# Optimization experiments

Hardware: AMD Instinct MI355X
Metric: run time of the kernel (lower is better)

## Reference

```python
import jax, jax.numpy as jnp
import numpy as np

DIST = 45
HID = 128
NLAYERS = 4
BATCH = 128


def _build_edges(d):
    n = d * d - 1
    sqrt_n = int(np.sqrt(n)) + 1
    src, dst = [], []
    for i in range(n):
        row, col = i // sqrt_n, i % sqrt_n
        for dr, dc in ((-1, 0), (1, 0), (0, -1), (0, 1)):
            nr, nc = row + dr, col + dc
            j = nr * sqrt_n + nc
            if 0 <= nr < sqrt_n and 0 <= j < n and j != i:
                src.append(i)
                dst.append(j)
    return np.asarray(src, np.int32), np.asarray(dst, np.int32), n


def setup_inputs() -> dict:
    key = jax.random.key(0)
    ks = jax.random.split(key, 8)
    src, dst, n = _build_edges(DIST)
    s = 1.0 / np.sqrt(HID)
    return {
        "x": jax.random.normal(ks[0], (BATCH, n), jnp.float32),
        "W_embed": jax.random.normal(ks[1], (1, HID), jnp.float32),
        "b_embed": jnp.zeros((HID,), jnp.float32),
        "gnn_W": jax.random.normal(ks[2], (NLAYERS, 2 * HID, HID), jnp.float32) * s,
        "gnn_b": jnp.zeros((NLAYERS, HID), jnp.float32),
        "ln_g": jnp.ones((NLAYERS, HID), jnp.float32),
        "ln_b": jnp.zeros((NLAYERS, HID), jnp.float32),
        "out_W1": jax.random.normal(ks[3], (HID, HID), jnp.float32) * s,
        "out_b1": jnp.zeros((HID,), jnp.float32),
        "out_W2": jax.random.normal(ks[4], (HID, 2), jnp.float32) * s,
        "out_b2": jnp.zeros((2,), jnp.float32),
        "edge_src": jnp.asarray(src),
        "edge_dst": jnp.asarray(dst),
    }


def _layer_norm(h, g, b, eps=1e-5):
    mu = h.mean(-1, keepdims=True)
    var = ((h - mu) ** 2).mean(-1, keepdims=True)
    return (h - mu) * jax.lax.rsqrt(var + eps) * g + b


def _segment_mean(h, src, dst, n_nodes):
    # h: [B, N, H] -> mean of incoming-neighbor features per node; 0 if no edge.
    hs = jnp.swapaxes(h[:, src, :], 0, 1)                 # [E, B, H]
    sums = jax.ops.segment_sum(hs, dst, num_segments=n_nodes)   # [N, B, H]
    cnt = jax.ops.segment_sum(jnp.ones_like(dst, jnp.float32), dst,
                              num_segments=n_nodes)              # [N]
    agg = jnp.where(cnt[:, None, None] > 0,
                    sums / jnp.maximum(cnt, 1.0)[:, None, None], 0.0)
    return jnp.swapaxes(agg, 0, 1)                        # [B, N, H]


def reference(x, W_embed, b_embed, gnn_W, gnn_b, ln_g, ln_b,
              out_W1, out_b1, out_W2, out_b2, edge_src, edge_dst):
    n_nodes = x.shape[1]
    # node_embed: Linear(1, H) applied to x[..., None]
    h = x[..., None] * W_embed[0] + b_embed               # [B, N, H]
    for l in range(gnn_W.shape[0]):
        agg = _segment_mean(h, edge_src, edge_dst, n_nodes)
        combined = jnp.concatenate([h, agg], axis=-1)     # [B, N, 2H]
        h = jax.nn.relu(combined @ gnn_W[l] + gnn_b[l])
        h = _layer_norm(h, ln_g[l], ln_b[l])
    graph_repr = h.mean(axis=1)                           # [B, H]
    hid = jax.nn.relu(graph_repr @ out_W1 + out_b1)
    return hid @ out_W2 + out_b2                          # [B, 2]
```

## Files before the change

### kernel.cpp

```cpp
#include <hip/hip_runtime.h>

typedef unsigned short u16;
typedef unsigned int   u32;
typedef __attribute__((ext_vector_type(8))) short short8;
typedef __attribute__((ext_vector_type(4))) float f32x4;

#define NN   2024
#define NB   128
#define HID  128
#define MT   128
#define MTOT (NN*NB)
#define NBLK (MTOT/MT)

__device__ __forceinline__ float bflo(u32 w){ union{u32 u; float f;}c; c.u=w<<16;        return c.f; }
__device__ __forceinline__ float bfhi(u32 w){ union{u32 u; float f;}c; c.u=w&0xffff0000u; return c.f; }
__device__ __forceinline__ float bf2f(u16 h){ union{u32 u; float f;}c; c.u=((u32)h)<<16; return c.f; }
__device__ __forceinline__ u16 f2bf(float f){ union{float f; u32 u;}c; c.f=f; return (u16)((c.u+0x7fffu+((c.u>>16)&1u))>>16); }
__device__ __forceinline__ u32 cvtpk(float lo, float hi){
  u32 r; asm("v_cvt_pk_bf16_f32 %0, %1, %2" : "=v"(r) : "v"(lo), "v"(hi)); return r;
}
__device__ __forceinline__ f32x4 mfma16(short8 a, short8 b, f32x4 c){
  return __builtin_amdgcn_mfma_f32_16x16x32_bf16(a,b,c,0,0,0);
}
__device__ __forceinline__ void glds16(const void* g, void* l){
  __builtin_amdgcn_global_load_lds((const __attribute__((address_space(1))) void*)g,
                                   (__attribute__((address_space(3))) void*)l, 16, 0, 0);
}

__device__ __forceinline__ short8 aggc(short8 a0, short8 a1, short8 a2, short8 a3,
                                       float w0, float w1, float w2, float w3){
  union{short8 s; u32 u[4];} A, B, C, D, R;
  A.s=a0; B.s=a1; C.s=a2; D.s=a3;
#pragma unroll
  for (int p=0;p<4;++p){
    float lo = w0*bflo(A.u[p]); lo = fmaf(w1,bflo(B.u[p]),lo); lo = fmaf(w2,bflo(C.u[p]),lo); lo = fmaf(w3,bflo(D.u[p]),lo);
    float hi = w0*bfhi(A.u[p]); hi = fmaf(w1,bfhi(B.u[p]),hi); hi = fmaf(w2,bfhi(C.u[p]),hi); hi = fmaf(w3,bfhi(D.u[p]),hi);
    R.u[p] = cvtpk(lo, hi);
  }
  return R.s;
}

__global__ __launch_bounds__(256, 2)
void layerG_k(const u16* __restrict__ hin, const u16* __restrict__ Wt,
              const float* __restrict__ bias, const float* __restrict__ lng,
              const float* __restrict__ lnb, u16* __restrict__ hout)
{
  __shared__ __align__(16) char lds[65536];
  char* Wl = lds;
  char* Ag = lds + 32768;

  const int t  = threadIdx.x;
  const int l  = t & 63;
  const int wv = t >> 6;
  const int wr = wv >> 1, wc = wv & 1;
  const int cB = l & 15, rg = l >> 4;

  const int orig = blockIdx.x;
  const int m0 = ((orig & 7)*253 + (orig >> 3)) * MT;

  const char* hb = (const char*)hin;

  {
#pragma unroll
    for (int i = 0; i < 8; ++i){
      const int slot = wv*8 + i;
      const int col  = slot*4 + (l >> 4);
      const u32 se   = (u32)col*256 + ((((u32)(l & 15))*8) ^ (((u32)(col & 7))<<3));
      glds16(Wt + se, Wl + (u32)slot*1024);
    }
  }

  const int r  = t >> 1;
  const int hf = t & 1;
  const int grow = m0 + r;
  const int nd = grow % NN;
  const int v0 = (nd >= 45), v1 = (nd <= NN-46), v2 = (nd >= 1), v3 = (nd <= NN-2);
  const int cnt = v0+v1+v2+v3;
  const float inv = (cnt==4) ? 0.25f : ((cnt==3) ? (1.f/3.f) : 0.5f);
  const float w0 = v0 ? inv : 0.f, w1 = v1 ? inv : 0.f;
  const float w2 = v2 ? inv : 0.f, w3 = v3 ? inv : 0.f;
  const u32 nb0 = (u32)(v0 ? grow-45 : grow)*256u + (u32)hf*128u;
  const u32 nb1 = (u32)(v1 ? grow+45 : grow)*256u + (u32)hf*128u;
  const u32 nb2 = (u32)(v2 ? grow-1  : grow)*256u + (u32)hf*128u;
  const u32 nb3 = (u32)(v3 ? grow+1  : grow)*256u + (u32)hf*128u;

  short8 nA[4], nB_[4], nC[4], nD[4];
#pragma unroll
  for (int c = 0; c < 4; ++c){
    nA[c]  = *(const short8*)(hb + nb0 + c*16);
    nB_[c] = *(const short8*)(hb + nb1 + c*16);
    nC[c]  = *(const short8*)(hb + nb2 + c*16);
    nD[c]  = *(const short8*)(hb + nb3 + c*16);
  }

  f32x4 acc[4][4];
#pragma unroll
  for (int m = 0; m < 4; ++m)
#pragma unroll
    for (int j = 0; j < 4; ++j)
      acc[m][j] = (f32x4){0.f,0.f,0.f,0.f};

  __syncthreads();

  const int c1 = t >> 1, hk = t & 1;
  short8 w1r[8];
  {
    const u16* s1p = Wt + (u32)c1*256 + 128 + (u32)hk*64;
#pragma unroll
    for (int i = 0; i < 8; ++i) w1r[i] = *(const short8*)(s1p + i*8);
  }

  const u32 kswz = ((u32)(cB & 7)) << 4;
  const char* wp[4];
#pragma unroll
  for (int j = 0; j < 4; ++j)
    wp[j] = Wl + (u32)(64*wc + 16*j + cB)*256;
  const char* selfp = hb + ((u32)(m0 + 64*wr + cB))*256u + (u32)rg*16;

#pragma unroll
  for (int ks = 0; ks < 4; ++ks){
    const u32 ka = ((u32)ks*64 + (u32)rg*16) ^ kswz;
    short8 wf[4];
#pragma unroll
    for (int j = 0; j < 4; ++j) wf[j] = *(const short8*)(wp[j] + ka);
#pragma unroll
    for (int m = 0; m < 4; ++m){
      short8 s = *(const short8*)(selfp + m*4096 + ks*64);
#pragma unroll
      for (int j = 0; j < 4; ++j) acc[m][j] = mfma16(s, wf[j], acc[m][j]);
    }
  }

  {
    char* arow = Ag + (u32)r*256;
    const u32 asw = ((u32)(r & 7)) << 4;
#pragma unroll
    for (int c = 0; c < 4; ++c){
      short8 v = aggc(nA[c], nB_[c], nC[c], nD[c], w0, w1, w2, w3);
      *(short8*)(arow + (((u32)(hf*128 + c*16)) ^ asw)) = v;
    }
    short8 mA[4], mB[4], mC[4], mD[4];
#pragma unroll
    for (int c = 0; c < 4; ++c){
      mA[c] = *(const short8*)(hb + nb0 + 64 + c*16);
      mB[c] = *(const short8*)(hb + nb1 + 64 + c*16);
      mC[c] = *(const short8*)(hb + nb2 + 64 + c*16);
      mD[c] = *(const short8*)(hb + nb3 + 64 + c*16);
    }
#pragma unroll
    for (int c = 0; c < 4; ++c){
      short8 v = aggc(mA[c], mB[c], mC[c], mD[c], w0, w1, w2, w3);
      *(short8*)(arow + (((u32)(hf*128 + 64 + c*16)) ^ asw)) = v;
    }
  }
  __syncthreads();

  {
    char* wdst = Wl + (u32)c1*256;
#pragma unroll
    for (int i = 0; i < 8; ++i)
      *(short8*)(wdst + (((u32)(hk*128 + i*16)) ^ (((u32)(c1 & 7))<<4))) = w1r[i];
  }
  __syncthreads();

  {
    const char* agp = Ag + (u32)(64*wr + cB)*256;
#pragma unroll
    for (int ks = 0; ks < 4; ++ks){
      const u32 ka = ((u32)ks*64 + (u32)rg*16) ^ kswz;
      short8 wf[4];
#pragma unroll
      for (int j = 0; j < 4; ++j) wf[j] = *(const short8*)(wp[j] + ka);
#pragma unroll
      for (int m = 0; m < 4; ++m){
        short8 a = *(const short8*)(agp + m*4096 + ka);
#pragma unroll
        for (int j = 0; j < 4; ++j) acc[m][j] = mfma16(a, wf[j], acc[m][j]);
      }
    }
  }
  __syncthreads();

  float2* red = (float2*)Wl;
  float b4[4], g4[4], bt4[4];
#pragma unroll
  for (int j = 0; j < 4; ++j){
    const int col = 64*wc + 16*j + cB;
    b4[j] = bias[col]; g4[j] = lng[col]; bt4[j] = lnb[col];
  }
#pragma unroll
  for (int m = 0; m < 4; ++m){
#pragma unroll
    for (int rr = 0; rr < 4; ++rr){
      float s1 = 0.f, s2 = 0.f;
#pragma unroll
      for (int j = 0; j < 4; ++j){
        float y = fmaxf(acc[m][j][rr] + b4[j], 0.f);
        acc[m][j][rr] = y;
        s1 += y; s2 = fmaf(y, y, s2);
      }
      s1 += __shfl_xor(s1,1); s1 += __shfl_xor(s1,2);
      s1 += __shfl_xor(s1,4); s1 += __shfl_xor(s1,8);
      s2 += __shfl_xor(s2,1); s2 += __shfl_xor(s2,2);
      s2 += __shfl_xor(s2,4); s2 += __shfl_xor(s2,8);
      if (cB == 0){
        const int rl = 64*wr + 16*m + 4*rg + rr;
        red[rl*2 + wc] = make_float2(s1, s2);
      }
    }
  }
  __syncthreads();

#pragma unroll
  for (int m = 0; m < 4; ++m){
#pragma unroll
    for (int rr = 0; rr < 4; ++rr){
      const int rl = 64*wr + 16*m + 4*rg + rr;
      const float2 A = red[rl*2], B = red[rl*2+1];
      const float s1 = A.x + B.x, s2 = A.y + B.y;
      const float muv = s1 * (1.f/128.f);
      const float var = s2 * (1.f/128.f) - muv*muv;
      const float rsv = rsqrtf(var + 1e-5f);
      const u32 sw = ((u32)(rl & 7)) << 4;
      char* rowp = Ag + (u32)rl*256;
#pragma unroll
      for (int j = 0; j < 4; ++j){
        const float y = fmaf((acc[m][j][rr]-muv)*rsv, g4[j], bt4[j]);
        const float p = __shfl_xor(y, 1);
        const u32 pk = (cB & 1) ? cvtpk(p, y) : cvtpk(y, p);
        const u32 off = ((u32)(128*wc + 32*j + 2*(cB & ~1))) ^ sw;
        *(u32*)(rowp + off) = pk;
      }
    }
  }
  __syncthreads();

  const int r2 = t >> 1, q2 = t & 1;
  const u32 sw2 = ((u32)(r2 & 7)) << 4;
  u16* dst = hout + (size_t)(m0 + r2)*HID + q2*64;
  const char* srow = Ag + (u32)r2*256;
#pragma unroll
  for (int i = 0; i < 8; ++i)
    *(short8*)(dst + i*8) = *(const short8*)(srow + (((u32)(q2*128 + i*16)) ^ sw2));
}

__global__ __launch_bounds__(256, 4)
void l1_k(const float* __restrict__ x, const float* __restrict__ uvec,
          const float* __restrict__ lng, const float* __restrict__ lnb,
          u16* __restrict__ hout)
{
  __shared__ float su[384];
  __shared__ float sg[128], sb[128];
  const int t = threadIdx.x;
  const int m0 = ((blockIdx.x & 7)*253 + (blockIdx.x >> 3)) * MT;
  for (int i = t; i < 384; i += 256) su[i] = uvec[i];
  if (t < 128){ sg[t] = lng[t]; sb[t] = lnb[t]; }
  __syncthreads();

  const int r = t >> 1, hf = t & 1;
  const int grow = m0 + r;
  const int nd = grow % NN;
  const int v0 = (nd >= 45), v1 = (nd <= NN-46), v2 = (nd >= 1), v3 = (nd <= NN-2);
  const int cnt = v0+v1+v2+v3;
  const float inv = (cnt==4) ? 0.25f : ((cnt==3) ? (1.f/3.f) : 0.5f);
  const float xv = x[grow];
  float mx = 0.f;
  if (v0) mx += x[grow-45];
  if (v1) mx += x[grow+45];
  if (v2) mx += x[grow-1];
  if (v3) mx += x[grow+1];
  mx *= inv;

  const int fb = hf*64;
  float4 yv[16];
  float s1 = 0.f, s2 = 0.f;
#pragma unroll
  for (int i = 0; i < 16; ++i){
    const float4 a = *(const float4*)(su + fb + i*4);
    const float4 b = *(const float4*)(su + 128 + fb + i*4);
    const float4 c = *(const float4*)(su + 256 + fb + i*4);
    float4 y;
    y.x = fmaxf(fmaf(xv, a.x, fmaf(mx, b.x, c.x)), 0.f);
    y.y = fmaxf(fmaf(xv, a.y, fmaf(mx, b.y, c.y)), 0.f);
    y.z = fmaxf(fmaf(xv, a.z, fmaf(mx, b.z, c.z)), 0.f);
    y.w = fmaxf(fmaf(xv, a.w, fmaf(mx, b.w, c.w)), 0.f);
    yv[i] = y;
    s1 += y.x + y.y + y.z + y.w;
    s2 = fmaf(y.x,y.x, fmaf(y.y,y.y, fmaf(y.z,y.z, fmaf(y.w,y.w, s2))));
  }
  s1 += __shfl_xor(s1, 1);
  s2 += __shfl_xor(s2, 1);
  const float muv = s1 * (1.f/128.f);
  const float var = s2 * (1.f/128.f) - muv*muv;
  const float rsv = rsqrtf(var + 1e-5f);

  u16* dst = hout + (size_t)grow*HID + fb;
#pragma unroll
  for (int i = 0; i < 8; ++i){
    const float4 ya = yv[2*i], yb = yv[2*i+1];
    const float4 ga = *(const float4*)(sg + fb + i*8);
    const float4 gb2 = *(const float4*)(sg + fb + i*8 + 4);
    const float4 ba = *(const float4*)(sb + fb + i*8);
    const float4 bb = *(const float4*)(sb + fb + i*8 + 4);
    u32 o0 = cvtpk(fmaf((ya.x-muv)*rsv, ga.x, ba.x), fmaf((ya.y-muv)*rsv, ga.y, ba.y));
    u32 o1 = cvtpk(fmaf((ya.z-muv)*rsv, ga.z, ba.z), fmaf((ya.w-muv)*rsv, ga.w, ba.w));
    u32 o2 = cvtpk(fmaf((yb.x-muv)*rsv, gb2.x, bb.x), fmaf((yb.y-muv)*rsv, gb2.y, bb.y));
    u32 o3 = cvtpk(fmaf((yb.z-muv)*rsv, gb2.z, bb.z), fmaf((yb.w-muv)*rsv, gb2.w, bb.w));
    uint4 pk = make_uint4(o0, o1, o2, o3);
    *(uint4*)(dst + i*8) = pk;
  }
}

__global__ void prep_k(const float* __restrict__ gw, u16* __restrict__ Wt){
  const int idx = blockIdx.x*256 + threadIdx.x;
  const int lay = idx >> 15;
  const int r   = idx & 32767;
  const int j   = r >> 8;
  const int k   = r & 255;
  Wt[idx] = f2bf(gw[lay*32768 + k*128 + j]);
}

__global__ void prep2_k(const float* __restrict__ We, const float* __restrict__ be,
                        const float* __restrict__ gW, const float* __restrict__ gb,
                        float* __restrict__ uvec){
  const int f = threadIdx.x;
  float u0 = 0.f, u1 = 0.f, c = 0.f;
  for (int k = 0; k < 128; ++k){
    const float a = gW[k*128 + f];
    const float b = gW[(128+k)*128 + f];
    u0 = fmaf(We[k], a, u0);
    u1 = fmaf(We[k], b, u1);
    c  = fmaf(be[k], a + b, c);
  }
  uvec[f] = u0; uvec[128+f] = u1; uvec[256+f] = c + gb[f];
}

__global__ void mean1_k(const u16* __restrict__ h, float* __restrict__ partial){
  __shared__ float red[16][16][8];
  const int blk = blockIdx.x;
  const int b = blk >> 3, s = blk & 7;
  const int t = threadIdx.x;
  const int cg = t & 15, q = t >> 4;
  const int nbeg = s*253, nend = nbeg + 253;
  float a[8] = {0.f,0.f,0.f,0.f,0.f,0.f,0.f,0.f};
  const u16* hb = h + (size_t)b * NN * HID;
  for (int n = nbeg + q; n < nend; n += 16){
    short8 v = *(const short8*)(hb + (size_t)n*HID + cg*8);
#pragma unroll
    for (int i = 0; i < 8; ++i) a[i] += bf2f((u16)v[i]);
  }
#pragma unroll
  for (int i = 0; i < 8; ++i) red[q][cg][i] = a[i];
  __syncthreads();
  if (t < 128){
    const int cc = t >> 3, i = t & 7;
    float v = 0.f;
#pragma unroll
    for (int qq = 0; qq < 16; ++qq) v += red[qq][cc][i];
    partial[((size_t)b*8 + s)*128 + t] = v;
  }
}

__global__ void mean2_k(const float* __restrict__ partial, float* __restrict__ gr){
  const int idx = blockIdx.x*256 + threadIdx.x;
  const int b = idx >> 7, c = idx & 127;
  float a = 0.f;
#pragma unroll
  for (int s = 0; s < 8; ++s) a += partial[((size_t)b*8 + s)*128 + c];
  gr[idx] = a * (1.0f / 2024.0f);
}

__global__ void head1_k(const float* __restrict__ gr, const float* __restrict__ W1,
                        const float* __restrict__ b1, float* __restrict__ hid){
  const int idx = blockIdx.x*256 + threadIdx.x;
  const int b = idx >> 7, j = idx & 127;
  const float* g = gr + b*128;
  float a = b1[j];
  for (int k = 0; k < 128; ++k) a = fmaf(g[k], W1[k*128 + j], a);
  hid[idx] = fmaxf(a, 0.f);
}

__global__ void head2_k(const float* __restrict__ hid, const float* __restrict__ W2,
                        const float* __restrict__ b2, float* __restrict__ out){
  const int t = threadIdx.x;
  const int b = t >> 1, o = t & 1;
  const float* hh = hid + b*128;
  float a = b2[o];
  for (int k = 0; k < 128; ++k) a = fmaf(hh[k], W2[k*2 + o], a);
  out[t] = a;
}

extern "C" void kernel_launch(void* const* d_in, const int* in_sizes, int n_in,
                              void* d_out, int out_size, void* d_ws, size_t ws_size,
                              hipStream_t stream){
  const float* x  = (const float*)d_in[0];
  const float* We = (const float*)d_in[1];
  const float* be = (const float*)d_in[2];
  const float* gW = (const float*)d_in[3];
  const float* gb = (const float*)d_in[4];
  const float* lg = (const float*)d_in[5];
  const float* lb = (const float*)d_in[6];
  const float* W1 = (const float*)d_in[7];
  const float* b1 = (const float*)d_in[8];
  const float* W2 = (const float*)d_in[9];
  const float* b2 = (const float*)d_in[10];
  float* out = (float*)d_out;

  char* w = (char*)d_ws;
  const size_t HB = (size_t)MTOT * HID * 2;
  u16*   hA   = (u16*)w;
  u16*   hB   = (u16*)(w + HB);
  u16*   Wt   = (u16*)(w + 2*HB);
  float* gr   = (float*)(w + 2*HB + 262144);
  float* hid  = (float*)(w + 2*HB + 262144 + 65536);
  float* uvec = (float*)(w + 2*HB + 262144 + 131072);
  float* partial = (float*)w;

  prep2_k<<<1, 128, 0, stream>>>(We, be, gW, gb, uvec);
  prep_k<<<512, 256, 0, stream>>>(gW, Wt);
  l1_k<<<NBLK, 256, 0, stream>>>(x, uvec, lg, lb, hA);
  layerG_k<<<NBLK, 256, 0, stream>>>(hA, Wt + 32768, gb + 128, lg + 128, lb + 128, hB);
  layerG_k<<<NBLK, 256, 0, stream>>>(hB, Wt + 65536, gb + 256, lg + 256, lb + 256, hA);
  layerG_k<<<NBLK, 256, 0, stream>>>(hA, Wt + 98304, gb + 384, lg + 384, lb + 384, hB);
  mean1_k<<<NB*8, 256, 0, stream>>>(hB, partial);
  mean2_k<<<64, 256, 0, stream>>>(partial, gr);
  head1_k<<<64, 256, 0, stream>>>(gr, W1, b1, hid);
  head2_k<<<1, 256, 0, stream>>>(hid, W2, b2, out);
}
```

Baseline: 381.8 us.

## Make GNN layer kernel persistent over 8 tiles with resident weights and prefetch

The per-layer kernel now processes eight 128-row tiles per block with 512 threads. The full 256x128 weight matrix is loaded once into LDS and reused across all tiles. Neighbor rows for the next tile are prefetched into registers while the current tile is computed, and the aggregation buffer is double-buffered. This cuts repeated weight loads and the mid-kernel weight swap, at the cost of more LDS per block (about 130KB) and fewer blocks (253), which may limit occupancy and load balance.

```diff
diff --git a/kernel.cpp b/kernel.cpp
--- a/kernel.cpp
+++ b/kernel.cpp
@@ -8,9 +8,11 @@
 #define NN   2024
 #define NB   128
 #define HID  128
-#define MT   128
 #define MTOT (NN*NB)
-#define NBLK (MTOT/MT)
+#define TILE 128
+#define TPB  8
+#define BROWS (TILE*TPB)
+#define NPBLK (MTOT/BROWS)
 
 __device__ __forceinline__ float bflo(u32 w){ union{u32 u; float f;}c; c.u=w<<16;        return c.f; }
 __device__ __forceinline__ float bfhi(u32 w){ union{u32 u; float f;}c; c.u=w&0xffff0000u; return c.f; }
@@ -26,222 +28,178 @@
   __builtin_amdgcn_global_load_lds((const __attribute__((address_space(1))) void*)g,
                                    (__attribute__((address_space(3))) void*)l, 16, 0, 0);
 }
-
-__device__ __forceinline__ short8 aggc(short8 a0, short8 a1, short8 a2, short8 a3,
-                                       float w0, float w1, float w2, float w3){
-  union{short8 s; u32 u[4];} A, B, C, D, R;
-  A.s=a0; B.s=a1; C.s=a2; D.s=a3;
-#pragma unroll
-  for (int p=0;p<4;++p){
-    float lo = w0*bflo(A.u[p]); lo = fmaf(w1,bflo(B.u[p]),lo); lo = fmaf(w2,bflo(C.u[p]),lo); lo = fmaf(w3,bflo(D.u[p]),lo);
-    float hi = w0*bfhi(A.u[p]); hi = fmaf(w1,bfhi(B.u[p]),hi); hi = fmaf(w2,bfhi(C.u[p]),hi); hi = fmaf(w3,bfhi(D.u[p]),hi);
-    R.u[p] = cvtpk(lo, hi);
-  }
-  return R.s;
-}
-
-__global__ __launch_bounds__(256, 2)
-void layerG_k(const u16* __restrict__ hin, const u16* __restrict__ Wt,
+__device__ __forceinline__ u32 agg1(u32 a, u32 b, u32 c, u32 d,
+                                    float w0, float w1, float w2, float w3){
+  float lo = w0*bflo(a); lo=fmaf(w1,bflo(b),lo); lo=fmaf(w2,bflo(c),lo); lo=fmaf(w3,bflo(d),lo);
+  float hi = w0*bfhi(a); hi=fmaf(w1,bfhi(b),hi); hi=fmaf(w2,bfhi(c),hi); hi=fmaf(w3,bfhi(d),hi);
+  return cvtpk(lo, hi);
+}
+
+__global__ __launch_bounds__(512, 2)
+void layerP_k(const u16* __restrict__ hin, const u16* __restrict__ Wt,
               const float* __restrict__ bias, const float* __restrict__ lng,
               const float* __restrict__ lnb, u16* __restrict__ hout)
 {
-  __shared__ __align__(16) char lds[65536];
-  char* Wl = lds;
-  char* Ag = lds + 32768;
+  __shared__ __align__(16) char Wl[65536];
+  __shared__ __align__(16) char Ag[2][32768];
+  __shared__ __align__(16) float2 red[128][4];
 
   const int t  = threadIdx.x;
   const int l  = t & 63;
   const int wv = t >> 6;
-  const int wr = wv >> 1, wc = wv & 1;
+  const int wr = wv & 1;
+  const int wc = wv >> 1;
   const int cB = l & 15, rg = l >> 4;
-
-  const int orig = blockIdx.x;
-  const int m0 = ((orig & 7)*253 + (orig >> 3)) * MT;
-
+  const int m0b = blockIdx.x * BROWS;
   const char* hb = (const char*)hin;
 
-  {
-#pragma unroll
-    for (int i = 0; i < 8; ++i){
-      const int slot = wv*8 + i;
-      const int col  = slot*4 + (l >> 4);
-      const u32 se   = (u32)col*256 + ((((u32)(l & 15))*8) ^ (((u32)(col & 7))<<3));
-      glds16(Wt + se, Wl + (u32)slot*1024);
-    }
-  }
-
-  const int r  = t >> 1;
-  const int hf = t & 1;
-  const int grow = m0 + r;
-  const int nd = grow % NN;
-  const int v0 = (nd >= 45), v1 = (nd <= NN-46), v2 = (nd >= 1), v3 = (nd <= NN-2);
-  const int cnt = v0+v1+v2+v3;
-  const float inv = (cnt==4) ? 0.25f : ((cnt==3) ? (1.f/3.f) : 0.5f);
-  const float w0 = v0 ? inv : 0.f, w1 = v1 ? inv : 0.f;
-  const float w2 = v2 ? inv : 0.f, w3 = v3 ? inv : 0.f;
-  const u32 nb0 = (u32)(v0 ? grow-45 : grow)*256u + (u32)hf*128u;
-  const u32 nb1 = (u32)(v1 ? grow+45 : grow)*256u + (u32)hf*128u;
-  const u32 nb2 = (u32)(v2 ? grow-1  : grow)*256u + (u32)hf*128u;
-  const u32 nb3 = (u32)(v3 ? grow+1  : grow)*256u + (u32)hf*128u;
-
-  short8 nA[4], nB_[4], nC[4], nD[4];
-#pragma unroll
-  for (int c = 0; c < 4; ++c){
-    nA[c]  = *(const short8*)(hb + nb0 + c*16);
-    nB_[c] = *(const short8*)(hb + nb1 + c*16);
-    nC[c]  = *(const short8*)(hb + nb2 + c*16);
-    nD[c]  = *(const short8*)(hb + nb3 + c*16);
-  }
-
-  f32x4 acc[4][4];
-#pragma unroll
-  for (int m = 0; m < 4; ++m)
-#pragma unroll
-    for (int j = 0; j < 4; ++j)
-      acc[m][j] = (f32x4){0.f,0.f,0.f,0.f};
+#pragma unroll
+  for (int i = 0; i < 8; ++i){
+    const int slot = wv*8 + i;
+    const int col  = slot*2 + (l >> 5);
+    const u32 kb   = ((u32)((l & 31)*16)) ^ ((u32)((col & 7) << 4));
+    glds16((const char*)Wt + (u32)col*512 + kb, Wl + (u32)slot*1024);
+  }
+
+  const int ar = t >> 2;
+  const int aq = t & 3;
+  const u32 qoff = (u32)aq * 64u;
+
+  uint4 nb0[4], nb1[4], nb2[4], nb3[4];
+  float wn0, wn1, wn2, wn3;
+  auto prefetch = [&](int it2){
+    const int rowg = m0b + it2*TILE + ar;
+    const int nd = rowg % NN;
+    const int v0 = (nd >= 45), v1 = (nd <= NN-46), v2 = (nd >= 1), v3 = (nd <= NN-2);
+    const int cnt = v0+v1+v2+v3;
+    const float inv = (cnt==4) ? 0.25f : ((cnt==3) ? (1.f/3.f) : 0.5f);
+    wn0 = v0?inv:0.f; wn1 = v1?inv:0.f; wn2 = v2?inv:0.f; wn3 = v3?inv:0.f;
+    const char* p0 = hb + (u32)(v0 ? rowg-45 : rowg)*256u + qoff;
+    const char* p1 = hb + (u32)(v1 ? rowg+45 : rowg)*256u + qoff;
+    const char* p2 = hb + (u32)(v2 ? rowg-1  : rowg)*256u + qoff;
+    const char* p3 = hb + (u32)(v3 ? rowg+1  : rowg)*256u + qoff;
+#pragma unroll
+    for (int c = 0; c < 4; ++c){
+      nb0[c] = *(const uint4*)(p0 + c*16);
+      nb1[c] = *(const uint4*)(p1 + c*16);
+      nb2[c] = *(const uint4*)(p2 + c*16);
+      nb3[c] = *(const uint4*)(p3 + c*16);
+    }
+  };
+  prefetch(0);
+
+  float bj[2], gj[2], btj[2];
+#pragma unroll
+  for (int j = 0; j < 2; ++j){
+    const int col = 32*wc + 16*j + cB;
+    bj[j] = bias[col]; gj[j] = lng[col]; btj[j] = lnb[col];
+  }
+  const u32 kswz = ((u32)(cB & 7)) << 4;
+  const char* wp0 = Wl + (u32)(32*wc + cB)*512;
+  const char* wp1 = Wl + (u32)(32*wc + 16 + cB)*512;
 
   __syncthreads();
 
-  const int c1 = t >> 1, hk = t & 1;
-  short8 w1r[8];
-  {
-    const u16* s1p = Wt + (u32)c1*256 + 128 + (u32)hk*64;
-#pragma unroll
-    for (int i = 0; i < 8; ++i) w1r[i] = *(const short8*)(s1p + i*8);
-  }
-
-  const u32 kswz = ((u32)(cB & 7)) << 4;
-  const char* wp[4];
-#pragma unroll
-  for (int j = 0; j < 4; ++j)
-    wp[j] = Wl + (u32)(64*wc + 16*j + cB)*256;
-  const char* selfp = hb + ((u32)(m0 + 64*wr + cB))*256u + (u32)rg*16;
-
-#pragma unroll
-  for (int ks = 0; ks < 4; ++ks){
-    const u32 ka = ((u32)ks*64 + (u32)rg*16) ^ kswz;
-    short8 wf[4];
-#pragma unroll
-    for (int j = 0; j < 4; ++j) wf[j] = *(const short8*)(wp[j] + ka);
+  for (int it = 0; it < TPB; ++it){
+    const int m0t = m0b + it*TILE;
+    char* agc = Ag[it & 1];
+
+    {
+      const float w0=wn0, w1=wn1, w2=wn2, w3=wn3;
+      char* arow = agc + (u32)ar*256;
+      const u32 sw = ((u32)(ar & 7)) << 4;
+#pragma unroll
+      for (int c = 0; c < 4; ++c){
+        uint4 v;
+        v.x = agg1(nb0[c].x, nb1[c].x, nb2[c].x, nb3[c].x, w0,w1,w2,w3);
+        v.y = agg1(nb0[c].y, nb1[c].y, nb2[c].y, nb3[c].y, w0,w1,w2,w3);
+        v.z = agg1(nb0[c].z, nb1[c].z, nb2[c].z, nb3[c].z, w0,w1,w2,w3);
+        v.w = agg1(nb0[c].w, nb1[c].w, nb2[c].w, nb3[c].w, w0,w1,w2,w3);
+        *(uint4*)(arow + ((qoff + (u32)c*16u) ^ sw)) = v;
+      }
+    }
+    if (it + 1 < TPB) prefetch(it + 1);
+
+    __syncthreads();
+
+    f32x4 acc[4][2];
+#pragma unroll
+    for (int m = 0; m < 4; ++m){ acc[m][0] = (f32x4){0,0,0,0}; acc[m][1] = (f32x4){0,0,0,0}; }
+
+    const char* selfp = hb  + ((u32)(m0t + 64*wr + cB))*256u;
+    const char* aggp  = agc + ((u32)(64*wr + cB))*256u;
+#pragma unroll
+    for (int ks = 0; ks < 4; ++ks){
+      const u32 kb = (u32)ks*64u + ((u32)rg)*16u;
+      const u32 kx = kb ^ kswz;
+      short8 w0a = *(const short8*)(wp0 + kx);
+      short8 w0b = *(const short8*)(wp1 + kx);
+      short8 w1a = *(const short8*)(wp0 + 256 + kx);
+      short8 w1b = *(const short8*)(wp1 + 256 + kx);
+#pragma unroll
+      for (int m = 0; m < 4; ++m){
+        short8 s = *(const short8*)(selfp + m*4096 + kb);
+        short8 a = *(const short8*)(aggp  + m*4096 + kx);
+        acc[m][0] = mfma16(s, w0a, acc[m][0]);
+        acc[m][1] = mfma16(s, w0b, acc[m][1]);
+        acc[m][0] = mfma16(a, w1a, acc[m][0]);
+        acc[m][1] = mfma16(a, w1b, acc[m][1]);
+      }
+    }
+
 #pragma unroll
     for (int m = 0; m < 4; ++m){
-      short8 s = *(const short8*)(selfp + m*4096 + ks*64);
-#pragma unroll
-      for (int j = 0; j < 4; ++j) acc[m][j] = mfma16(s, wf[j], acc[m][j]);
-    }
-  }
-
-  {
-    char* arow = Ag + (u32)r*256;
-    const u32 asw = ((u32)(r & 7)) << 4;
-#pragma unroll
-    for (int c = 0; c < 4; ++c){
-      short8 v = aggc(nA[c], nB_[c], nC[c], nD[c], w0, w1, w2, w3);
-      *(short8*)(arow + (((u32)(hf*128 + c*16)) ^ asw)) = v;
-    }
-    short8 mA[4], mB[4], mC[4], mD[4];
-#pragma unroll
-    for (int c = 0; c < 4; ++c){
-      mA[c] = *(const short8*)(hb + nb0 + 64 + c*16);
-      mB[c] = *(const short8*)(hb + nb1 + 64 + c*16);
-      mC[c] = *(const short8*)(hb + nb2 + 64 + c*16);
-      mD[c] = *(const short8*)(hb + nb3 + 64 + c*16);
-    }
-#pragma unroll
-    for (int c = 0; c < 4; ++c){
-      short8 v = aggc(mA[c], mB[c], mC[c], mD[c], w0, w1, w2, w3);
-      *(short8*)(arow + (((u32)(hf*128 + 64 + c*16)) ^ asw)) = v;
-    }
-  }
-  __syncthreads();
-
-  {
-    char* wdst = Wl + (u32)c1*256;
-#pragma unroll
-    for (int i = 0; i < 8; ++i)
-      *(short8*)(wdst + (((u32)(hk*128 + i*16)) ^ (((u32)(c1 & 7))<<4))) = w1r[i];
-  }
-  __syncthreads();
-
-  {
-    const char* agp = Ag + (u32)(64*wr + cB)*256;
-#pragma unroll
-    for (int ks = 0; ks < 4; ++ks){
-      const u32 ka = ((u32)ks*64 + (u32)rg*16) ^ kswz;
-      short8 wf[4];
-#pragma unroll
-      for (int j = 0; j < 4; ++j) wf[j] = *(const short8*)(wp[j] + ka);
-#pragma unroll
-      for (int m = 0; m < 4; ++m){
-        short8 a = *(const short8*)(agp + m*4096 + ka);
-#pragma unroll
-        for (int j = 0; j < 4; ++j) acc[m][j] = mfma16(a, wf[j], acc[m][j]);
+#pragma unroll
+      for (int rr = 0; rr < 4; ++rr){
+        float y0 = fmaxf(acc[m][0][rr] + bj[0], 0.f);
+        float y1 = fmaxf(acc[m][1][rr] + bj[1], 0.f);
+        acc[m][0][rr] = y0; acc[m][1][rr] = y1;
+        float s1 = y0 + y1;
+        float s2 = fmaf(y0, y0, y1*y1);
+        s1 += __shfl_xor(s1,1); s2 += __shfl_xor(s2,1);
+        s1 += __shfl_xor(s1,2); s2 += __shfl_xor(s2,2);
+        s1 += __shfl_xor(s1,4); s2 += __shfl_xor(s2,4);
+        s1 += __shfl_xor(s1,8); s2 += __shfl_xor(s2,8);
+        if (cB == 0) red[64*wr + 16*m + 4*rg + rr][wc] = make_float2(s1, s2);
       }
     }
-  }
-  __syncthreads();
-
-  float2* red = (float2*)Wl;
-  float b4[4], g4[4], bt4[4];
-#pragma unroll
-  for (int j = 0; j < 4; ++j){
-    const int col = 64*wc + 16*j + cB;
-    b4[j] = bias[col]; g4[j] = lng[col]; bt4[j] = lnb[col];
-  }
-#pragma unroll
-  for (int m = 0; m < 4; ++m){
-#pragma unroll
-    for (int rr = 0; rr < 4; ++rr){
-      float s1 = 0.f, s2 = 0.f;
-#pragma unroll
-      for (int j = 0; j < 4; ++j){
-        float y = fmaxf(acc[m][j][rr] + b4[j], 0.f);
-        acc[m][j][rr] = y;
-        s1 += y; s2 = fmaf(y, y, s2);
+    __syncthreads();
+
+#pragma unroll
+    for (int m = 0; m < 4; ++m){
+#pragma unroll
+      for (int rr = 0; rr < 4; ++rr){
+        const int row = 64*wr + 16*m + 4*rg + rr;
+        const float4 A = *(const float4*)&red[row][0];
+        const float4 B = *(const float4*)&red[row][2];
+        const float s1 = A.x + A.z + B.x + B.z;
+        const float s2 = A.y + A.w + B.y + B.w;
+        const float mu = s1 * (1.f/128.f);
+        const float va = s2 * (1.f/128.f) - mu*mu;
+        const float rs = rsqrtf(va + 1e-5f);
+        const u32 sw = ((u32)(row & 7)) << 4;
+        char* rowp = agc + (u32)row*256;
+#pragma unroll
+        for (int j = 0; j < 2; ++j){
+          const float y = fmaf((acc[m][j][rr]-mu)*rs, gj[j], btj[j]);
+          const float p = __shfl_xor(y, 1);
+          const u32 pk = (cB & 1) ? cvtpk(p, y) : cvtpk(y, p);
+          const u32 off = ((u32)(64*wc + 32*j + 2*(cB & ~1))) ^ sw;
+          *(u32*)(rowp + off) = pk;
+        }
       }
-      s1 += __shfl_xor(s1,1); s1 += __shfl_xor(s1,2);
-      s1 += __shfl_xor(s1,4); s1 += __shfl_xor(s1,8);
-      s2 += __shfl_xor(s2,1); s2 += __shfl_xor(s2,2);
-      s2 += __shfl_xor(s2,4); s2 += __shfl_xor(s2,8);
-      if (cB == 0){
-        const int rl = 64*wr + 16*m + 4*rg + rr;
-        red[rl*2 + wc] = make_float2(s1, s2);
-      }
-    }
-  }
-  __syncthreads();
-
-#pragma unroll
-  for (int m = 0; m < 4; ++m){
-#pragma unroll
-    for (int rr = 0; rr < 4; ++rr){
-      const int rl = 64*wr + 16*m + 4*rg + rr;
-      const float2 A = red[rl*2], B = red[rl*2+1];
-      const float s1 = A.x + B.x, s2 = A.y + B.y;
-      const float muv = s1 * (1.f/128.f);
-      const float var = s2 * (1.f/128.f) - muv*muv;
-      const float rsv = rsqrtf(var + 1e-5f);
-      const u32 sw = ((u32)(rl & 7)) << 4;
-      char* rowp = Ag + (u32)rl*256;
-#pragma unroll
-      for (int j = 0; j < 4; ++j){
-        const float y = fmaf((acc[m][j][rr]-muv)*rsv, g4[j], bt4[j]);
-        const float p = __shfl_xor(y, 1);
-        const u32 pk = (cB & 1) ? cvtpk(p, y) : cvtpk(y, p);
-        const u32 off = ((u32)(128*wc + 32*j + 2*(cB & ~1))) ^ sw;
-        *(u32*)(rowp + off) = pk;
-      }
-    }
-  }
-  __syncthreads();
-
-  const int r2 = t >> 1, q2 = t & 1;
-  const u32 sw2 = ((u32)(r2 & 7)) << 4;
-  u16* dst = hout + (size_t)(m0 + r2)*HID + q2*64;
-  const char* srow = Ag + (u32)r2*256;
-#pragma unroll
-  for (int i = 0; i < 8; ++i)
-    *(short8*)(dst + i*8) = *(const short8*)(srow + (((u32)(q2*128 + i*16)) ^ sw2));
+    }
+    __syncthreads();
+
+    {
+      const u32 sw2 = ((u32)(ar & 7)) << 4;
+      const char* srow = agc + (u32)ar*256;
+      u16* dst = hout + (size_t)(m0t + ar)*HID + aq*32;
+#pragma unroll
+      for (int i = 0; i < 4; ++i)
+        *(short8*)(dst + i*8) = *(const short8*)(srow + ((qoff + (u32)i*16u) ^ sw2));
+    }
+  }
 }
 
 __global__ __launch_bounds__(256, 4)
@@ -252,7 +210,7 @@
   __shared__ float su[384];
   __shared__ float sg[128], sb[128];
   const int t = threadIdx.x;
-  const int m0 = ((blockIdx.x & 7)*253 + (blockIdx.x >> 3)) * MT;
+  const int m0 = ((blockIdx.x & 7)*253 + (blockIdx.x >> 3)) * 128;
   for (int i = t; i < 384; i += 256) su[i] = uvec[i];
   if (t < 128){ sg[t] = lng[t]; sb[t] = lnb[t]; }
   __syncthreads();
@@ -418,10 +376,10 @@
 
   prep2_k<<<1, 128, 0, stream>>>(We, be, gW, gb, uvec);
   prep_k<<<512, 256, 0, stream>>>(gW, Wt);
-  l1_k<<<NBLK, 256, 0, stream>>>(x, uvec, lg, lb, hA);
-  layerG_k<<<NBLK, 256, 0, stream>>>(hA, Wt + 32768, gb + 128, lg + 128, lb + 128, hB);
-  layerG_k<<<NBLK, 256, 0, stream>>>(hB, Wt + 65536, gb + 256, lg + 256, lb + 256, hA);
-  layerG_k<<<NBLK, 256, 0, stream>>>(hA, Wt + 98304, gb + 384, lg + 384, lb + 384, hB);
+  l1_k<<<MTOT/128, 256, 0, stream>>>(x, uvec, lg, lb, hA);
+  layerP_k<<<NPBLK, 512, 0, stream>>>(hA, Wt + 32768, gb + 128, lg + 128, lb + 128, hB);
+  layerP_k<<<NPBLK, 512, 0, stream>>>(hB, Wt + 65536, gb + 256, lg + 256, lb + 256, hA);
+  layerP_k<<<NPBLK, 512, 0, stream>>>(hA, Wt + 98304, gb + 384, lg + 384, lb + 384, hB);
   mean1_k<<<NB*8, 256, 0, stream>>>(hB, partial);
   mean2_k<<<64, 256, 0, stream>>>(partial, gr);
   head1_k<<<64, 256, 0, stream>>>(gr, W1, b1, hid);
```

Result: slower. 398.1 us (+4.3%).

## Split neighbor aggregation into separate kernel and compute GEMM in place

Applied to the files above, without the earlier changes.

The fused layer kernel used to gather four neighbors, compute the mean and write it to LDS before the second half of the GEMM. It is now split in two: a standalone aggregation kernel writes the aggregated features to global memory, and a GEMM+LayerNorm kernel with 512 threads and 256-row tiles loads the full 256-wide weight matrix into LDS once and reads self and aggregated rows directly from global. The layer output overwrites h in place, with one buffer for h and one for the aggregate. This removes the mid-kernel weight reload and two barriers, but adds an extra global write and read of the aggregate per layer plus three more kernel launches.

```diff
diff --git a/kernel.cpp b/kernel.cpp
--- a/kernel.cpp
+++ b/kernel.cpp
@@ -8,9 +8,9 @@
 #define NN   2024
 #define NB   128
 #define HID  128
-#define MT   128
 #define MTOT (NN*NB)
-#define NBLK (MTOT/MT)
+#define RPB  256
+#define NPB  (MTOT/RPB)
 
 __device__ __forceinline__ float bflo(u32 w){ union{u32 u; float f;}c; c.u=w<<16;        return c.f; }
 __device__ __forceinline__ float bfhi(u32 w){ union{u32 u; float f;}c; c.u=w&0xffff0000u; return c.f; }
@@ -26,29 +26,52 @@
   __builtin_amdgcn_global_load_lds((const __attribute__((address_space(1))) void*)g,
                                    (__attribute__((address_space(3))) void*)l, 16, 0, 0);
 }
-
-__device__ __forceinline__ short8 aggc(short8 a0, short8 a1, short8 a2, short8 a3,
-                                       float w0, float w1, float w2, float w3){
-  union{short8 s; u32 u[4];} A, B, C, D, R;
-  A.s=a0; B.s=a1; C.s=a2; D.s=a3;
-#pragma unroll
-  for (int p=0;p<4;++p){
-    float lo = w0*bflo(A.u[p]); lo = fmaf(w1,bflo(B.u[p]),lo); lo = fmaf(w2,bflo(C.u[p]),lo); lo = fmaf(w3,bflo(D.u[p]),lo);
-    float hi = w0*bfhi(A.u[p]); hi = fmaf(w1,bfhi(B.u[p]),hi); hi = fmaf(w2,bfhi(C.u[p]),hi); hi = fmaf(w3,bfhi(D.u[p]),hi);
-    R.u[p] = cvtpk(lo, hi);
-  }
-  return R.s;
-}
-
-__global__ __launch_bounds__(256, 2)
-void layerG_k(const u16* __restrict__ hin, const u16* __restrict__ Wt,
-              const float* __restrict__ bias, const float* __restrict__ lng,
-              const float* __restrict__ lnb, u16* __restrict__ hout)
+__device__ __forceinline__ u32 agg1(u32 a, u32 b, u32 c, u32 d,
+                                    float w0, float w1, float w2, float w3){
+  float lo = w0*bflo(a); lo=fmaf(w1,bflo(b),lo); lo=fmaf(w2,bflo(c),lo); lo=fmaf(w3,bflo(d),lo);
+  float hi = w0*bfhi(a); hi=fmaf(w1,bfhi(b),hi); hi=fmaf(w2,bfhi(c),hi); hi=fmaf(w3,bfhi(d),hi);
+  return cvtpk(lo, hi);
+}
+
+__global__ __launch_bounds__(256, 4)
+void aggA_k(const u16* __restrict__ h, u16* __restrict__ a)
 {
-  __shared__ __align__(16) char lds[65536];
-  char* Wl = lds;
-  char* Ag = lds + 32768;
-
+  const int t = threadIdx.x;
+  const int row = blockIdx.x*128 + (t >> 1);
+  const int hf = t & 1;
+  const int nd = row % NN;
+  const int v0 = (nd >= 45), v1 = (nd <= NN-46), v2 = (nd >= 1), v3 = (nd <= NN-2);
+  const int cnt = v0+v1+v2+v3;
+  const float inv = (cnt==4) ? 0.25f : ((cnt==3) ? (1.f/3.f) : 0.5f);
+  const float w0 = v0?inv:0.f, w1 = v1?inv:0.f, w2 = v2?inv:0.f, w3 = v3?inv:0.f;
+
+  const u16* p0 = h + (u32)(v0 ? row-45 : row)*128u + hf*64;
+  const u16* p1 = h + (u32)(v1 ? row+45 : row)*128u + hf*64;
+  const u16* p2 = h + (u32)(v2 ? row-1  : row)*128u + hf*64;
+  const u16* p3 = h + (u32)(v3 ? row+1  : row)*128u + hf*64;
+  u16* dst = a + (u32)row*128u + hf*64;
+
+#pragma unroll
+  for (int c = 0; c < 8; ++c){
+    union{ uint4 v; u32 u[4]; } b0, b1, b2, b3, o;
+    b0.v = *(const uint4*)(p0 + c*8);
+    b1.v = *(const uint4*)(p1 + c*8);
+    b2.v = *(const uint4*)(p2 + c*8);
+    b3.v = *(const uint4*)(p3 + c*8);
+#pragma unroll
+    for (int p = 0; p < 4; ++p)
+      o.u[p] = agg1(b0.u[p], b1.u[p], b2.u[p], b3.u[p], w0, w1, w2, w3);
+    *(uint4*)(dst + c*8) = o.v;
+  }
+}
+
+__global__ __launch_bounds__(512, 2)
+void layerB_k(u16* __restrict__ h, const u16* __restrict__ a,
+              const u16* __restrict__ Wt, const float* __restrict__ bias,
+              const float* __restrict__ lng, const float* __restrict__ lnb)
+{
+  __shared__ __align__(16) char Wl[65536];
+  __shared__ __align__(16) float2 red[256][2];
   const int t  = threadIdx.x;
   const int l  = t & 63;
   const int wv = t >> 6;
@@ -56,41 +79,15 @@
   const int cB = l & 15, rg = l >> 4;
 
   const int orig = blockIdx.x;
-  const int m0 = ((orig & 7)*253 + (orig >> 3)) * MT;
-
-  const char* hb = (const char*)hin;
-
-  {
-#pragma unroll
-    for (int i = 0; i < 8; ++i){
-      const int slot = wv*8 + i;
-      const int col  = slot*4 + (l >> 4);
-      const u32 se   = (u32)col*256 + ((((u32)(l & 15))*8) ^ (((u32)(col & 7))<<3));
-      glds16(Wt + se, Wl + (u32)slot*1024);
-    }
-  }
-
-  const int r  = t >> 1;
-  const int hf = t & 1;
-  const int grow = m0 + r;
-  const int nd = grow % NN;
-  const int v0 = (nd >= 45), v1 = (nd <= NN-46), v2 = (nd >= 1), v3 = (nd <= NN-2);
-  const int cnt = v0+v1+v2+v3;
-  const float inv = (cnt==4) ? 0.25f : ((cnt==3) ? (1.f/3.f) : 0.5f);
-  const float w0 = v0 ? inv : 0.f, w1 = v1 ? inv : 0.f;
-  const float w2 = v2 ? inv : 0.f, w3 = v3 ? inv : 0.f;
-  const u32 nb0 = (u32)(v0 ? grow-45 : grow)*256u + (u32)hf*128u;
-  const u32 nb1 = (u32)(v1 ? grow+45 : grow)*256u + (u32)hf*128u;
-  const u32 nb2 = (u32)(v2 ? grow-1  : grow)*256u + (u32)hf*128u;
-  const u32 nb3 = (u32)(v3 ? grow+1  : grow)*256u + (u32)hf*128u;
-
-  short8 nA[4], nB_[4], nC[4], nD[4];
-#pragma unroll
-  for (int c = 0; c < 4; ++c){
-    nA[c]  = *(const short8*)(hb + nb0 + c*16);
-    nB_[c] = *(const short8*)(hb + nb1 + c*16);
-    nC[c]  = *(const short8*)(hb + nb2 + c*16);
-    nD[c]  = *(const short8*)(hb + nb3 + c*16);
+  const int xcd = orig & 7, bx = orig >> 3;
+  const int m0 = ((xcd < 4 ? xcd*127 : 508 + (xcd-4)*126) + bx) * RPB;
+
+#pragma unroll
+  for (int i = 0; i < 8; ++i){
+    const int slot = wv*8 + i;
+    const int col  = slot*2 + (l >> 5);
+    const u32 kb   = ((u32)((l & 31)*16)) ^ ((u32)((col & 7) << 4));
+    glds16((const char*)Wt + (u32)col*512 + kb, Wl + (u32)slot*1024);
   }
 
   f32x4 acc[4][4];
@@ -100,88 +97,45 @@
     for (int j = 0; j < 4; ++j)
       acc[m][j] = (f32x4){0.f,0.f,0.f,0.f};
 
-  __syncthreads();
-
-  const int c1 = t >> 1, hk = t & 1;
-  short8 w1r[8];
-  {
-    const u16* s1p = Wt + (u32)c1*256 + 128 + (u32)hk*64;
-#pragma unroll
-    for (int i = 0; i < 8; ++i) w1r[i] = *(const short8*)(s1p + i*8);
-  }
-
   const u32 kswz = ((u32)(cB & 7)) << 4;
   const char* wp[4];
 #pragma unroll
   for (int j = 0; j < 4; ++j)
-    wp[j] = Wl + (u32)(64*wc + 16*j + cB)*256;
-  const char* selfp = hb + ((u32)(m0 + 64*wr + cB))*256u + (u32)rg*16;
+    wp[j] = Wl + (u32)(64*wc + 16*j + cB)*512;
+  const char* sp = (const char*)h + (u32)(m0 + 64*wr + cB)*256u + (u32)rg*16u;
+  const char* ap = (const char*)a + (u32)(m0 + 64*wr + cB)*256u + (u32)rg*16u;
+
+  __syncthreads();
 
 #pragma unroll
   for (int ks = 0; ks < 4; ++ks){
-    const u32 ka = ((u32)ks*64 + (u32)rg*16) ^ kswz;
+    const u32 kb = (u32)ks*64u + (u32)rg*16u;
+    const u32 kx = kb ^ kswz;
     short8 wf[4];
 #pragma unroll
-    for (int j = 0; j < 4; ++j) wf[j] = *(const short8*)(wp[j] + ka);
+    for (int j = 0; j < 4; ++j) wf[j] = *(const short8*)(wp[j] + kx);
 #pragma unroll
     for (int m = 0; m < 4; ++m){
-      short8 s = *(const short8*)(selfp + m*4096 + ks*64);
+      short8 s = *(const short8*)(sp + m*4096 + ks*64);
 #pragma unroll
       for (int j = 0; j < 4; ++j) acc[m][j] = mfma16(s, wf[j], acc[m][j]);
     }
   }
-
-  {
-    char* arow = Ag + (u32)r*256;
-    const u32 asw = ((u32)(r & 7)) << 4;
-#pragma unroll
-    for (int c = 0; c < 4; ++c){
-      short8 v = aggc(nA[c], nB_[c], nC[c], nD[c], w0, w1, w2, w3);
-      *(short8*)(arow + (((u32)(hf*128 + c*16)) ^ asw)) = v;
+#pragma unroll
+  for (int ks = 0; ks < 4; ++ks){
+    const u32 kb = (u32)ks*64u + (u32)rg*16u;
+    const u32 kx = (256u + kb) ^ kswz;
+    short8 wf[4];
+#pragma unroll
+    for (int j = 0; j < 4; ++j) wf[j] = *(const short8*)(wp[j] + kx);
+#pragma unroll
+    for (int m = 0; m < 4; ++m){
+      short8 v = *(const short8*)(ap + m*4096 + ks*64);
+#pragma unroll
+      for (int j = 0; j < 4; ++j) acc[m][j] = mfma16(v, wf[j], acc[m][j]);
     }
-    short8 mA[4], mB[4], mC[4], mD[4];
-#pragma unroll
-    for (int c = 0; c < 4; ++c){
-      mA[c] = *(const short8*)(hb + nb0 + 64 + c*16);
-      mB[c] = *(const short8*)(hb + nb1 + 64 + c*16);
-      mC[c] = *(const short8*)(hb + nb2 + 64 + c*16);
-      mD[c] = *(const short8*)(hb + nb3 + 64 + c*16);
-    }
-#pragma unroll
-    for (int c = 0; c < 4; ++c){
-      short8 v = aggc(mA[c], mB[c], mC[c], mD[c], w0, w1, w2, w3);
-      *(short8*)(arow + (((u32)(hf*128 + 64 + c*16)) ^ asw)) = v;
-    }
-  }
-  __syncthreads();
-
-  {
-    char* wdst = Wl + (u32)c1*256;
-#pragma unroll
-    for (int i = 0; i < 8; ++i)
-      *(short8*)(wdst + (((u32)(hk*128 + i*16)) ^ (((u32)(c1 & 7))<<4))) = w1r[i];
-  }
-  __syncthreads();
-
-  {
-    const char* agp = Ag + (u32)(64*wr + cB)*256;
-#pragma unroll
-    for (int ks = 0; ks < 4; ++ks){
-      const u32 ka = ((u32)ks*64 + (u32)rg*16) ^ kswz;
-      short8 wf[4];
-#pragma unroll
-      for (int j = 0; j < 4; ++j) wf[j] = *(const short8*)(wp[j] + ka);
-#pragma unroll
-      for (int m = 0; m < 4; ++m){
-        short8 a = *(const short8*)(agp + m*4096 + ka);
-#pragma unroll
-        for (int j = 0; j < 4; ++j) acc[m][j] = mfma16(a, wf[j], acc[m][j]);
-      }
-    }
-  }
-  __syncthreads();
-
-  float2* red = (float2*)Wl;
+  }
+
   float b4[4], g4[4], bt4[4];
 #pragma unroll
   for (int j = 0; j < 4; ++j){
@@ -203,29 +157,27 @@
       s1 += __shfl_xor(s1,4); s1 += __shfl_xor(s1,8);
       s2 += __shfl_xor(s2,1); s2 += __shfl_xor(s2,2);
       s2 += __shfl_xor(s2,4); s2 += __shfl_xor(s2,8);
-      if (cB == 0){
-        const int rl = 64*wr + 16*m + 4*rg + rr;
-        red[rl*2 + wc] = make_float2(s1, s2);
-      }
+      if (cB == 0) red[64*wr + 16*m + 4*rg + rr][wc] = make_float2(s1, s2);
     }
   }
   __syncthreads();
 
+  char* trB = Wl;
 #pragma unroll
   for (int m = 0; m < 4; ++m){
 #pragma unroll
     for (int rr = 0; rr < 4; ++rr){
       const int rl = 64*wr + 16*m + 4*rg + rr;
-      const float2 A = red[rl*2], B = red[rl*2+1];
+      const float2 A = red[rl][0], B = red[rl][1];
       const float s1 = A.x + B.x, s2 = A.y + B.y;
-      const float muv = s1 * (1.f/128.f);
-      const float var = s2 * (1.f/128.f) - muv*muv;
-      const float rsv = rsqrtf(var + 1e-5f);
+      const float mu = s1 * (1.f/128.f);
+      const float va = s2 * (1.f/128.f) - mu*mu;
+      const float rs = rsqrtf(va + 1e-5f);
       const u32 sw = ((u32)(rl & 7)) << 4;
-      char* rowp = Ag + (u32)rl*256;
+      char* rowp = trB + (u32)rl*256;
 #pragma unroll
       for (int j = 0; j < 4; ++j){
-        const float y = fmaf((acc[m][j][rr]-muv)*rsv, g4[j], bt4[j]);
+        const float y = fmaf((acc[m][j][rr]-mu)*rs, g4[j], bt4[j]);
         const float p = __shfl_xor(y, 1);
         const u32 pk = (cB & 1) ? cvtpk(p, y) : cvtpk(y, p);
         const u32 off = ((u32)(128*wc + 32*j + 2*(cB & ~1))) ^ sw;
@@ -235,13 +187,13 @@
   }
   __syncthreads();
 
-  const int r2 = t >> 1, q2 = t & 1;
-  const u32 sw2 = ((u32)(r2 & 7)) << 4;
-  u16* dst = hout + (size_t)(m0 + r2)*HID + q2*64;
-  const char* srow = Ag + (u32)r2*256;
+  const int r = t >> 1, q = t & 1;
+  const u32 sw2 = ((u32)(r & 7)) << 4;
+  u16* dst = h + (size_t)(m0 + r)*HID + q*64;
+  const char* srow = trB + (u32)r*256;
 #pragma unroll
   for (int i = 0; i < 8; ++i)
-    *(short8*)(dst + i*8) = *(const short8*)(srow + (((u32)(q2*128 + i*16)) ^ sw2));
+    *(short8*)(dst + i*8) = *(const short8*)(srow + (((u32)(q*128 + i*16)) ^ sw2));
 }
 
 __global__ __launch_bounds__(256, 4)
@@ -252,7 +204,7 @@
   __shared__ float su[384];
   __shared__ float sg[128], sb[128];
   const int t = threadIdx.x;
-  const int m0 = ((blockIdx.x & 7)*253 + (blockIdx.x >> 3)) * MT;
+  const int m0 = ((blockIdx.x & 7)*253 + (blockIdx.x >> 3)) * 128;
   for (int i = t; i < 384; i += 256) su[i] = uvec[i];
   if (t < 128){ sg[t] = lng[t]; sb[t] = lnb[t]; }
   __syncthreads();
@@ -276,14 +228,14 @@
   float s1 = 0.f, s2 = 0.f;
 #pragma unroll
   for (int i = 0; i < 16; ++i){
-    const float4 a = *(const float4*)(su + fb + i*4);
-    const float4 b = *(const float4*)(su + 128 + fb + i*4);
-    const float4 c = *(const float4*)(su + 256 + fb + i*4);
+    const float4 aa = *(const float4*)(su + fb + i*4);
+    const float4 bb = *(const float4*)(su + 128 + fb + i*4);
+    const float4 cc = *(const float4*)(su + 256 + fb + i*4);
     float4 y;
-    y.x = fmaxf(fmaf(xv, a.x, fmaf(mx, b.x, c.x)), 0.f);
-    y.y = fmaxf(fmaf(xv, a.y, fmaf(mx, b.y, c.y)), 0.f);
-    y.z = fmaxf(fmaf(xv, a.z, fmaf(mx, b.z, c.z)), 0.f);
-    y.w = fmaxf(fmaf(xv, a.w, fmaf(mx, b.w, c.w)), 0.f);
+    y.x = fmaxf(fmaf(xv, aa.x, fmaf(mx, bb.x, cc.x)), 0.f);
+    y.y = fmaxf(fmaf(xv, aa.y, fmaf(mx, bb.y, cc.y)), 0.f);
+    y.z = fmaxf(fmaf(xv, aa.z, fmaf(mx, bb.z, cc.z)), 0.f);
+    y.w = fmaxf(fmaf(xv, aa.w, fmaf(mx, bb.w, cc.w)), 0.f);
     yv[i] = y;
     s1 += y.x + y.y + y.z + y.w;
     s2 = fmaf(y.x,y.x, fmaf(y.y,y.y, fmaf(y.z,y.z, fmaf(y.w,y.w, s2))));
@@ -408,21 +360,26 @@
 
   char* w = (char*)d_ws;
   const size_t HB = (size_t)MTOT * HID * 2;
-  u16*   hA   = (u16*)w;
-  u16*   hB   = (u16*)(w + HB);
+  u16*   h    = (u16*)w;
+  u16*   a    = (u16*)(w + HB);
   u16*   Wt   = (u16*)(w + 2*HB);
-  float* gr   = (float*)(w + 2*HB + 262144);
-  float* hid  = (float*)(w + 2*HB + 262144 + 65536);
-  float* uvec = (float*)(w + 2*HB + 262144 + 131072);
-  float* partial = (float*)w;
+  float* uvec = (float*)(w + 2*HB + 262144);
+  float* gr   = (float*)(w + 2*HB + 266240);
+  float* hid  = (float*)(w + 2*HB + 331776);
+  float* partial = (float*)(w + HB);
 
   prep2_k<<<1, 128, 0, stream>>>(We, be, gW, gb, uvec);
   prep_k<<<512, 256, 0, stream>>>(gW, Wt);
-  l1_k<<<NBLK, 256, 0, stream>>>(x, uvec, lg, lb, hA);
-  layerG_k<<<NBLK, 256, 0, stream>>>(hA, Wt + 32768, gb + 128, lg + 128, lb + 128, hB);
-  layerG_k<<<NBLK, 256, 0, stream>>>(hB, Wt + 65536, gb + 256, lg + 256, lb + 256, hA);
-  layerG_k<<<NBLK, 256, 0, stream>>>(hA, Wt + 98304, gb + 384, lg + 384, lb + 384, hB);
-  mean1_k<<<NB*8, 256, 0, stream>>>(hB, partial);
+  l1_k<<<MTOT/128, 256, 0, stream>>>(x, uvec, lg, lb, h);
+
+  aggA_k<<<MTOT/128, 256, 0, stream>>>(h, a);
+  layerB_k<<<NPB, 512, 0, stream>>>(h, a, Wt + 32768, gb + 128, lg + 128, lb + 128);
+  aggA_k<<<MTOT/128, 256, 0, stream>>>(h, a);
+  layerB_k<<<NPB, 512, 0, stream>>>(h, a, Wt + 65536, gb + 256, lg + 256, lb + 256);
+  aggA_k<<<MTOT/128, 256, 0, stream>>>(h, a);
+  layerB_k<<<NPB, 512, 0, stream>>>(h, a, Wt + 98304, gb + 384, lg + 384, lb + 384);
+
+  mean1_k<<<NB*8, 256, 0, stream>>>(h, partial);
   mean2_k<<<64, 256, 0, stream>>>(partial, gr);
   head1_k<<<64, 256, 0, stream>>>(gr, W1, b1, hid);
   head2_k<<<1, 256, 0, stream>>>(hid, W2, b2, out);
```

Result: slower. 547.7 us (+43.5%).
